# Performance work log

Hardware: AMD Instinct MI355X
Metric: run time of the kernel (lower is better)

The kernel has to match this reference:

```python
import jax, jax.numpy as jnp
import numpy as np

N_NODES = 50000
N_EDGES = 800000
VOCAB = 15000
IN_FEATS = 128
HIDDEN = 32
HEADS = 4
N_GRAPHS = 64
NEG_SLOPE = 0.2


def setup_inputs() -> dict:
    key = jax.random.key(0)
    ks = jax.random.split(key, 16)
    word_ids = jax.random.randint(ks[0], (N_NODES,), 0, VOCAB)
    edge_src = jax.random.randint(ks[1], (N_EDGES,), 0, N_NODES)
    edge_dst = jax.random.randint(ks[2], (N_EDGES,), 0, N_NODES)
    node_graph_id = jnp.sort(jax.random.randint(ks[3], (N_NODES,), 0, N_GRAPHS))
    y_data = jax.random.uniform(ks[4], (N_GRAPHS,))
    word_embeds = jax.random.normal(ks[5], (VOCAB, IN_FEATS)) * 0.02
    W0 = jax.random.normal(ks[6], (IN_FEATS, HEADS * HIDDEN)) * (1.0 / np.sqrt(IN_FEATS))
    al0 = jax.random.normal(ks[7], (HEADS, HIDDEN)) * 0.1
    ar0 = jax.random.normal(ks[8], (HEADS, HIDDEN)) * 0.1
    W1 = jax.random.normal(ks[9], (HEADS * HIDDEN, HEADS * HIDDEN)) * (1.0 / np.sqrt(HEADS * HIDDEN))
    al1 = jax.random.normal(ks[10], (HEADS, HIDDEN)) * 0.1
    ar1 = jax.random.normal(ks[11], (HEADS, HIDDEN)) * 0.1
    out_w = jax.random.normal(ks[12], (HEADS * HIDDEN, 1)) * (1.0 / np.sqrt(HEADS * HIDDEN))
    out_b = jnp.zeros((1,))
    return {"word_ids": word_ids, "edge_src": edge_src, "edge_dst": edge_dst,
            "node_graph_id": node_graph_id, "y_data": y_data,
            "word_embeds": word_embeds, "W0": W0, "al0": al0, "ar0": ar0,
            "W1": W1, "al1": al1, "ar1": ar1, "out_w": out_w, "out_b": out_b}


def gat_layer(h, src, dst, W, al, ar):
    # h: [N, Fin] -> feat: [N, H, D]
    feat = (h @ W).reshape(N_NODES, HEADS, HIDDEN)
    el = (feat * al[None]).sum(-1)  # [N, H]
    er = (feat * ar[None]).sum(-1)  # [N, H]
    e = jax.nn.leaky_relu(el[src] + er[dst], NEG_SLOPE)  # [E, H]
    # segment softmax over incoming edges of each dst node
    m = jax.ops.segment_max(e, dst, num_segments=N_NODES)
    m = jnp.where(jnp.isfinite(m), m, 0.0)
    ex = jnp.exp(e - m[dst])
    denom = jax.ops.segment_sum(ex, dst, num_segments=N_NODES)
    alpha = ex / (denom[dst] + 1e-10)  # [E, H]
    msg = feat[src] * alpha[:, :, None]  # [E, H, D]
    out = jax.ops.segment_sum(msg, dst, num_segments=N_NODES)  # [N, H, D]
    return jax.nn.elu(out).reshape(N_NODES, HEADS * HIDDEN)


def reference(word_ids, edge_src, edge_dst, node_graph_id, y_data,
              word_embeds, W0, al0, ar0, W1, al1, ar1, out_w, out_b):
    h = word_embeds[word_ids]  # [N, IN_FEATS]
    h = gat_layer(h, edge_src, edge_dst, W0, al0, ar0)
    h = gat_layer(h, edge_src, edge_dst, W1, al1, ar1)
    # per-graph max pooling over nodes
    pooled = jax.ops.segment_max(h, node_graph_id, num_segments=N_GRAPHS)
    pooled = jnp.where(jnp.isfinite(pooled), pooled, 0.0)  # guard empty graphs
    logits = (pooled @ out_w + out_b).reshape(-1)  # [G]
    # BCE with logits (stable)
    loss = jnp.mean(jnp.maximum(logits, 0.0) - logits * y_data
                    + jnp.log1p(jnp.exp(-jnp.abs(logits))))
    y_pred = jax.nn.sigmoid(logits)[:, None]
    return (loss, y_pred)
```

## Files before the change

kernel.cpp:

```cpp
#include <hip/hip_runtime.h>
#include <math.h>

#define N_NODES 50000
#define N_EDGES 800000
#define HEADS 4
#define N_GRAPHS 64
#define NEG_SLOPE 0.2f
#define LOG2E 1.4426950408889634f
#define SCAN_NB 196
#define POOL_CHUNK 200
#define POOL_NB 250
#define FEAT_NB 1563
#define EDGE_Q 200000
#define EDGE_NB 782

__device__ __forceinline__ unsigned fkey(float f) {
    unsigned u = __float_as_uint(f);
    return (u & 0x80000000u) ? ~u : (u | 0x80000000u);
}
__device__ __forceinline__ float kval(unsigned k) {
    unsigned u = (k & 0x80000000u) ? (k & 0x7FFFFFFFu) : ~k;
    return __uint_as_float(u);
}

__device__ __forceinline__ unsigned short f2bf(float f) {
    unsigned u = __float_as_uint(f);
    u += 0x7FFFu + ((u >> 16) & 1u);
    return (unsigned short)(u >> 16);
}
__device__ __forceinline__ unsigned pack_bf2(float a, float b) {
    return (unsigned)f2bf(a) | ((unsigned)f2bf(b) << 16);
}


__global__ void hist_kernel(const int* __restrict__ dst, int* __restrict__ deg,
                            int* __restrict__ rank) {
    int i = blockIdx.x * 256 + threadIdx.x;
    if (i >= EDGE_Q) return;
    int e0 = i, e1 = i + EDGE_Q, e2 = i + 2 * EDGE_Q, e3 = i + 3 * EDGE_Q;
    int d0 = dst[e0], d1 = dst[e1], d2 = dst[e2], d3 = dst[e3];
    int r0 = atomicAdd(&deg[d0], 1);
    int r1 = atomicAdd(&deg[d1], 1);
    int r2 = atomicAdd(&deg[d2], 1);
    int r3 = atomicAdd(&deg[d3], 1);
    rank[e0] = r0; rank[e1] = r1; rank[e2] = r2; rank[e3] = r3;
}

__global__ void partial_kernel(const int* __restrict__ deg, int* __restrict__ partial) {
    int t = threadIdx.x, b = blockIdx.x;
    int i = b * 256 + t;
    int v = (i < N_NODES) ? deg[i] : 0;
    #pragma unroll
    for (int off = 1; off < 64; off <<= 1) v += __shfl_xor(v, off, 64);
    __shared__ int wsum[4];
    if ((t & 63) == 0) wsum[t >> 6] = v;
    __syncthreads();
    if (t == 0) partial[b] = wsum[0] + wsum[1] + wsum[2] + wsum[3];
}

__global__ void csr_offsets_kernel(const int* __restrict__ deg, const int* __restrict__ partial,
                                   int* __restrict__ row_start) {
    __shared__ int sb[SCAN_NB];
    __shared__ int wsumA[4];
    __shared__ int wsumB[4];
    int t = threadIdx.x, b = blockIdx.x;
    int lane = t & 63, w = t >> 6;
    {
        int v = (t < SCAN_NB) ? partial[t] : 0;
        int incl = v;
        #pragma unroll
        for (int off = 1; off < 64; off <<= 1) {
            int u = __shfl_up(incl, off, 64);
            if (lane >= off) incl += u;
        }
        if (lane == 63) wsumA[w] = incl;
        __syncthreads();
        int woff = 0;
        #pragma unroll
        for (int k = 0; k < 4; ++k) if (k < w) woff += wsumA[k];
        if (t < SCAN_NB) sb[t] = woff + incl - v;
        __syncthreads();
    }
    int i = b * 256 + t;
    int v = (i < N_NODES) ? deg[i] : 0;
    int incl = v;
    #pragma unroll
    for (int off = 1; off < 64; off <<= 1) {
        int u = __shfl_up(incl, off, 64);
        if (lane >= off) incl += u;
    }
    if (lane == 63) wsumB[w] = incl;
    __syncthreads();
    int woff = sb[b];
    #pragma unroll
    for (int k = 0; k < 4; ++k) if (k < w) woff += wsumB[k];
    int excl = woff + incl - v;
    if (i < N_NODES) row_start[i] = excl;
    else if (i == N_NODES) row_start[i] = excl;
}

__global__ void scatter_kernel(const int* __restrict__ src, const int* __restrict__ dst,
                               const int* __restrict__ rank, const int* __restrict__ row_start,
                               int* __restrict__ csr_src) {
    int i = blockIdx.x * 256 + threadIdx.x;
    if (i >= EDGE_Q) return;
    int e0 = i, e1 = i + EDGE_Q, e2 = i + 2 * EDGE_Q, e3 = i + 3 * EDGE_Q;
    int d0 = dst[e0], d1 = dst[e1], d2 = dst[e2], d3 = dst[e3];
    int k0 = rank[e0], k1 = rank[e1], k2 = rank[e2], k3 = rank[e3];
    int s0 = src[e0], s1 = src[e1], s2 = src[e2], s3 = src[e3];
    int p0 = row_start[d0] + k0;
    int p1 = row_start[d1] + k1;
    int p2 = row_start[d2] + k2;
    int p3 = row_start[d3] + k3;
    csr_src[p0] = s0;
    csr_src[p1] = s1;
    csr_src[p2] = s2;
    csr_src[p3] = s3;
}


__global__ __launch_bounds__(256, 2)
void feat_kernel(const float* __restrict__ h, const int* __restrict__ wid,
                 const float* __restrict__ W,
                 const float* __restrict__ al, const float* __restrict__ ar,
                 unsigned* __restrict__ featb, float* __restrict__ el,
                 float* __restrict__ er) {
    __shared__ float Wl[128 * 128];
    __shared__ float hl[32 * 128];
    int t = threadIdx.x;
    {
        const float4* W4 = (const float4*)W;
        float4* Wl4 = (float4*)Wl;
        #pragma unroll
        for (int i = 0; i < 16; ++i) Wl4[t + 256 * i] = W4[t + 256 * i];
    }
    int n0 = blockIdx.x * 32;
    {
        const float4* h4 = (const float4*)h;
        float4* hl4 = (float4*)hl;
        #pragma unroll
        for (int r = 0; r < 4; ++r) {
            int i = t + 256 * r;
            int n = i >> 5, q = i & 31;
            float4 v = {0.f, 0.f, 0.f, 0.f};
            int gn = n0 + n;
            if (gn < N_NODES) {
                int row = wid ? wid[gn] : gn;
                v = h4[(size_t)row * 32 + q];
            }
            hl4[n * 32 + q] = v;
        }
    }
    __syncthreads();
    int ng = t >> 5, cg = t & 31;
    const float4* hl4 = (const float4*)hl;
    const float4* Wl4 = (const float4*)Wl;
    float4 acc[4];
    #pragma unroll
    for (int i = 0; i < 4; ++i) acc[i] = {0.f, 0.f, 0.f, 0.f};
    for (int k4 = 0; k4 < 32; ++k4) {
        float4 a0 = hl4[(ng * 4 + 0) * 32 + k4];
        float4 a1 = hl4[(ng * 4 + 1) * 32 + k4];
        float4 a2 = hl4[(ng * 4 + 2) * 32 + k4];
        float4 a3 = hl4[(ng * 4 + 3) * 32 + k4];
        #pragma unroll
        for (int kk = 0; kk < 4; ++kk) {
            float4 w = Wl4[(k4 * 4 + kk) * 32 + cg];
            float c0 = ((const float*)&a0)[kk];
            float c1 = ((const float*)&a1)[kk];
            float c2 = ((const float*)&a2)[kk];
            float c3 = ((const float*)&a3)[kk];
            acc[0].x += c0 * w.x; acc[0].y += c0 * w.y; acc[0].z += c0 * w.z; acc[0].w += c0 * w.w;
            acc[1].x += c1 * w.x; acc[1].y += c1 * w.y; acc[1].z += c1 * w.z; acc[1].w += c1 * w.w;
            acc[2].x += c2 * w.x; acc[2].y += c2 * w.y; acc[2].z += c2 * w.z; acc[2].w += c2 * w.w;
            acc[3].x += c3 * w.x; acc[3].y += c3 * w.y; acc[3].z += c3 * w.z; acc[3].w += c3 * w.w;
        }
    }
    int hd = cg >> 3;
    float a0v = al[cg * 4], a1v = al[cg * 4 + 1], a2v = al[cg * 4 + 2], a3v = al[cg * 4 + 3];
    float r0v = ar[cg * 4], r1v = ar[cg * 4 + 1], r2v = ar[cg * 4 + 2], r3v = ar[cg * 4 + 3];
    #pragma unroll
    for (int i = 0; i < 4; ++i) {
        int n = n0 + ng * 4 + i;
        if (n >= N_NODES) break;
        uint2 pk;
        pk.x = pack_bf2(acc[i].x, acc[i].y);
        pk.y = pack_bf2(acc[i].z, acc[i].w);
        *(uint2*)(featb + (size_t)n * 64 + cg * 2) = pk;
        float pl = acc[i].x * a0v + acc[i].y * a1v + acc[i].z * a2v + acc[i].w * a3v;
        float pr = acc[i].x * r0v + acc[i].y * r1v + acc[i].z * r2v + acc[i].w * r3v;
        #pragma unroll
        for (int off = 1; off < 8; off <<= 1) {
            pl += __shfl_xor(pl, off, 64);
            pr += __shfl_xor(pr, off, 64);
        }
        if ((t & 7) == 0) {
            el[n * 4 + hd] = pl * LOG2E;
            er[n * 4 + hd] = pr * LOG2E;
        }
    }
}

__global__ void gat_aggregate(const int* __restrict__ row_start, const int* __restrict__ csr_src,
                              const unsigned* __restrict__ featb, const float* __restrict__ el,
                              const float* __restrict__ er, float* __restrict__ hout) {
    int lane = threadIdx.x & 63;
    int d = blockIdx.x * 4 + (threadIdx.x >> 6);
    int beg = row_start[d], end = row_start[d + 1];
    int eg = lane >> 4;
    int li = lane & 15;
    int hc = li >> 2;
    float er_h = er[d * 4 + hc];
    float a0 = 0.f, a1 = 0.f, a2 = 0.f, a3 = 0.f;
    float a4 = 0.f, a5 = 0.f, a6 = 0.f, a7 = 0.f;
    float dsum = 0.f;
    int b8 = beg + ((end - beg) & ~7);
    for (int base = beg; base < b8; base += 8) {
        int ea = base + eg, eb = base + 4 + eg;
        int sa = csr_src[ea];
        int sb = csr_src[eb];
        float la = el[sa * 4 + hc];
        float lb = el[sb * 4 + hc];
        uint4 pa = *(const uint4*)(featb + (size_t)sa * 64 + li * 4);
        uint4 pb = *(const uint4*)(featb + (size_t)sb * 64 + li * 4);
        float va = la + er_h; va = fmaxf(va, NEG_SLOPE * va);
        float vb = lb + er_h; vb = fmaxf(vb, NEG_SLOPE * vb);
        float xa = exp2f(va), xb = exp2f(vb);
        dsum += xa + xb;
        a0 += __uint_as_float(pa.x << 16) * xa;
        a1 += __uint_as_float(pa.x & 0xFFFF0000u) * xa;
        a2 += __uint_as_float(pa.y << 16) * xa;
        a3 += __uint_as_float(pa.y & 0xFFFF0000u) * xa;
        a4 += __uint_as_float(pa.z << 16) * xa;
        a5 += __uint_as_float(pa.z & 0xFFFF0000u) * xa;
        a6 += __uint_as_float(pa.w << 16) * xa;
        a7 += __uint_as_float(pa.w & 0xFFFF0000u) * xa;
        a0 += __uint_as_float(pb.x << 16) * xb;
        a1 += __uint_as_float(pb.x & 0xFFFF0000u) * xb;
        a2 += __uint_as_float(pb.y << 16) * xb;
        a3 += __uint_as_float(pb.y & 0xFFFF0000u) * xb;
        a4 += __uint_as_float(pb.z << 16) * xb;
        a5 += __uint_as_float(pb.z & 0xFFFF0000u) * xb;
        a6 += __uint_as_float(pb.w << 16) * xb;
        a7 += __uint_as_float(pb.w & 0xFFFF0000u) * xb;
    }
    for (int ee = b8 + eg; ee < end; ee += 4) {
        int s = csr_src[ee];
        float lv = el[s * 4 + hc];
        uint4 pv = *(const uint4*)(featb + (size_t)s * 64 + li * 4);
        float v = lv + er_h; v = fmaxf(v, NEG_SLOPE * v);
        float x = exp2f(v);
        dsum += x;
        a0 += __uint_as_float(pv.x << 16) * x;
        a1 += __uint_as_float(pv.x & 0xFFFF0000u) * x;
        a2 += __uint_as_float(pv.y << 16) * x;
        a3 += __uint_as_float(pv.y & 0xFFFF0000u) * x;
        a4 += __uint_as_float(pv.z << 16) * x;
        a5 += __uint_as_float(pv.z & 0xFFFF0000u) * x;
        a6 += __uint_as_float(pv.w << 16) * x;
        a7 += __uint_as_float(pv.w & 0xFFFF0000u) * x;
    }
    #pragma unroll
    for (int off = 16; off < 64; off <<= 1) {
        a0 += __shfl_xor(a0, off, 64);
        a1 += __shfl_xor(a1, off, 64);
        a2 += __shfl_xor(a2, off, 64);
        a3 += __shfl_xor(a3, off, 64);
        a4 += __shfl_xor(a4, off, 64);
        a5 += __shfl_xor(a5, off, 64);
        a6 += __shfl_xor(a6, off, 64);
        a7 += __shfl_xor(a7, off, 64);
        dsum += __shfl_xor(dsum, off, 64);
    }
    if (eg == 0) {
        float inv = 1.f / (dsum + 1e-10f);
        float o0 = a0 * inv, o1 = a1 * inv, o2 = a2 * inv, o3 = a3 * inv;
        float o4 = a4 * inv, o5 = a5 * inv, o6 = a6 * inv, o7 = a7 * inv;
        o0 = o0 > 0.f ? o0 : expm1f(o0);
        o1 = o1 > 0.f ? o1 : expm1f(o1);
        o2 = o2 > 0.f ? o2 : expm1f(o2);
        o3 = o3 > 0.f ? o3 : expm1f(o3);
        o4 = o4 > 0.f ? o4 : expm1f(o4);
        o5 = o5 > 0.f ? o5 : expm1f(o5);
        o6 = o6 > 0.f ? o6 : expm1f(o6);
        o7 = o7 > 0.f ? o7 : expm1f(o7);
        float4* op = (float4*)(hout + (size_t)d * 128);
        float4 w0 = {o0, o1, o2, o3};
        float4 w1 = {o4, o5, o6, o7};
        op[li * 2] = w0;
        op[li * 2 + 1] = w1;
    }
}


__global__ void pool_kernel(const int* __restrict__ gid, const float* __restrict__ h,
                            unsigned* __restrict__ pkeys) {
    int t = threadIdx.x;
    int c = t & 127;
    int par = t >> 7;
    int n0 = blockIdx.x * POOL_CHUNK;
    float m = 0.f;
    int cur_g = -1;
    for (int n = n0 + par; n < n0 + POOL_CHUNK; n += 2) {
        int g = gid[n];
        if (g != cur_g) {
            if (cur_g >= 0) atomicMax(&pkeys[cur_g * 128 + c], fkey(m));
            cur_g = g;
            m = -3.0e38f;
        }
        m = fmaxf(m, h[(size_t)n * 128 + c]);
    }
    if (cur_g >= 0) atomicMax(&pkeys[cur_g * 128 + c], fkey(m));
}

__global__ void logits_kernel(const unsigned* __restrict__ pkeys, const float* __restrict__ w,
                              const float* __restrict__ bptr, float* __restrict__ logits) {
    int g = blockIdx.x, t = threadIdx.x;
    float sum = 0.f;
    for (int c = t; c < 128; c += 64) {
        unsigned k = pkeys[g * 128 + c];
        float v = (k == 0u) ? 0.f : kval(k);
        sum += v * w[c];
    }
    #pragma unroll
    for (int off = 32; off; off >>= 1) sum += __shfl_down(sum, off, 64);
    if (t == 0) logits[g] = sum + bptr[0];
}

__global__ void final_kernel(const float* __restrict__ logits, const float* __restrict__ y,
                             float* __restrict__ out) {
    int t = threadIdx.x;
    float l = logits[t];
    float term = fmaxf(l, 0.f) - l * y[t] + log1pf(expf(-fabsf(l)));
    float s = term;
    #pragma unroll
    for (int off = 32; off; off >>= 1) s += __shfl_down(s, off, 64);
    out[1 + t] = 1.f / (1.f + expf(-l));
    if (t == 0) out[0] = s * (1.f / 64.f);
}

extern "C" void kernel_launch(void* const* d_in, const int* in_sizes, int n_in,
                              void* d_out, int out_size, void* d_ws, size_t ws_size,
                              hipStream_t stream) {
    const int* word_ids  = (const int*)d_in[0];
    const int* esrc      = (const int*)d_in[1];
    const int* edst      = (const int*)d_in[2];
    const int* gid       = (const int*)d_in[3];
    const float* y_data  = (const float*)d_in[4];
    const float* emb     = (const float*)d_in[5];
    const float* W0      = (const float*)d_in[6];
    const float* al0     = (const float*)d_in[7];
    const float* ar0     = (const float*)d_in[8];
    const float* W1      = (const float*)d_in[9];
    const float* al1     = (const float*)d_in[10];
    const float* ar1     = (const float*)d_in[11];
    const float* out_w   = (const float*)d_in[12];
    const float* out_b   = (const float*)d_in[13];
    float* out = (float*)d_out;

    float* ws = (float*)d_ws;
    unsigned* featb  = (unsigned*)ws;
    float*    hbuf   = ws + 3200000;
    float*    el     = ws + 9600000;
    float*    er     = ws + 9800000;
    int*      row_st = (int*)(ws + 10000000);
    int*      deg    = (int*)(ws + 10051000);
    int*      rank   = (int*)(ws + 10101000);
    int*      csrsrc = (int*)(ws + 10901000);
    int*      partial= (int*)(ws + 11701000);
    unsigned* pkeys  = (unsigned*)(ws + 11701400);
    float*    logits = ws + 11709592;

    hipMemsetAsync(deg, 0, (size_t)N_NODES * 4, stream);
    hist_kernel<<<EDGE_NB, 256, 0, stream>>>(edst, deg, rank);
    partial_kernel<<<SCAN_NB, 256, 0, stream>>>(deg, partial);
    csr_offsets_kernel<<<SCAN_NB, 256, 0, stream>>>(deg, partial, row_st);
    scatter_kernel<<<EDGE_NB, 256, 0, stream>>>(esrc, edst, rank, row_st, csrsrc);

    feat_kernel<<<FEAT_NB, 256, 0, stream>>>(emb, word_ids, W0, al0, ar0, featb, el, er);
    gat_aggregate<<<12500, 256, 0, stream>>>(row_st, csrsrc, featb, el, er, hbuf);
    feat_kernel<<<FEAT_NB, 256, 0, stream>>>(hbuf, nullptr, W1, al1, ar1, featb, el, er);
    gat_aggregate<<<12500, 256, 0, stream>>>(row_st, csrsrc, featb, el, er, hbuf);

    hipMemsetAsync(pkeys, 0, (size_t)N_GRAPHS * 128 * 4, stream);
    pool_kernel<<<POOL_NB, 256, 0, stream>>>(gid, hbuf, pkeys);
    logits_kernel<<<N_GRAPHS, 64, 0, stream>>>(pkeys, out_w, out_b, logits);
    final_kernel<<<1, 64, 0, stream>>>(logits, y_data, out);
}
```

Baseline: 329.4 us.

## Compute GAT feature projection with bf16 MFMA using pre-packed weight fragments

Replaces the FP32 FMA matmul in feat_kernel with bf16 MFMA 16x16x32 instructions. A small wfrag_kernel first repacks W into bf16 fragment order, so the feature kernel no longer stages the full 64KB FP32 weight matrix in LDS for every block. Each block now handles 64 nodes and fewer blocks are launched. Node features are also rounded to bf16 before the multiply, which lowers precision, and the el/er head reductions are reworked to fit the MFMA output layout.

```diff
diff --git a/kernel.cpp b/kernel.cpp
--- a/kernel.cpp
+++ b/kernel.cpp
@@ -10,9 +10,12 @@
 #define SCAN_NB 196
 #define POOL_CHUNK 200
 #define POOL_NB 250
-#define FEAT_NB 1563
+#define FEAT_NB 782
 #define EDGE_Q 200000
 #define EDGE_NB 782
+
+typedef __attribute__((ext_vector_type(8))) short bf16x8;
+typedef __attribute__((ext_vector_type(4))) float f32x4;
 
 __device__ __forceinline__ unsigned fkey(float f) {
     unsigned u = __float_as_uint(f);
@@ -108,95 +111,105 @@
     int d0 = dst[e0], d1 = dst[e1], d2 = dst[e2], d3 = dst[e3];
     int k0 = rank[e0], k1 = rank[e1], k2 = rank[e2], k3 = rank[e3];
     int s0 = src[e0], s1 = src[e1], s2 = src[e2], s3 = src[e3];
-    int p0 = row_start[d0] + k0;
-    int p1 = row_start[d1] + k1;
-    int p2 = row_start[d2] + k2;
-    int p3 = row_start[d3] + k3;
-    csr_src[p0] = s0;
-    csr_src[p1] = s1;
-    csr_src[p2] = s2;
-    csr_src[p3] = s3;
-}
-
-
-__global__ __launch_bounds__(256, 2)
+    csr_src[row_start[d0] + k0] = s0;
+    csr_src[row_start[d1] + k1] = s1;
+    csr_src[row_start[d2] + k2] = s2;
+    csr_src[row_start[d3] + k3] = s3;
+}
+
+
+__global__ void wfrag_kernel(const float* __restrict__ W, unsigned* __restrict__ wf) {
+    int slot = blockIdx.x * 256 + threadIdx.x;
+    int f = slot >> 6, l = slot & 63;
+    int n = l & 15, q = l >> 4;
+    int ct = f >> 2, kq = f & 3;
+    int col = 16 * ct + n;
+    int k0 = 32 * kq + 8 * q;
+    uint4 o;
+    o.x = pack_bf2(W[(k0 + 0) * 128 + col], W[(k0 + 1) * 128 + col]);
+    o.y = pack_bf2(W[(k0 + 2) * 128 + col], W[(k0 + 3) * 128 + col]);
+    o.z = pack_bf2(W[(k0 + 4) * 128 + col], W[(k0 + 5) * 128 + col]);
+    o.w = pack_bf2(W[(k0 + 6) * 128 + col], W[(k0 + 7) * 128 + col]);
+    ((uint4*)wf)[slot] = o;
+}
+
+__global__ __launch_bounds__(256)
 void feat_kernel(const float* __restrict__ h, const int* __restrict__ wid,
-                 const float* __restrict__ W,
+                 const unsigned* __restrict__ wf,
                  const float* __restrict__ al, const float* __restrict__ ar,
                  unsigned* __restrict__ featb, float* __restrict__ el,
                  float* __restrict__ er) {
-    __shared__ float Wl[128 * 128];
-    __shared__ float hl[32 * 128];
+    __shared__ unsigned hl[64 * 68];
     int t = threadIdx.x;
-    {
-        const float4* W4 = (const float4*)W;
-        float4* Wl4 = (float4*)Wl;
+    int n0 = blockIdx.x * 64;
+    const float4* h4 = (const float4*)h;
+    #pragma unroll
+    for (int r = 0; r < 8; ++r) {
+        int i = t + 256 * r;
+        int n = i >> 5, q4 = i & 31;
+        float4 v = {0.f, 0.f, 0.f, 0.f};
+        int gn = n0 + n;
+        if (gn < N_NODES) {
+            int row = wid ? wid[gn] : gn;
+            v = h4[(size_t)row * 32 + q4];
+        }
+        hl[n * 68 + q4 * 2]     = pack_bf2(v.x, v.y);
+        hl[n * 68 + q4 * 2 + 1] = pack_bf2(v.z, v.w);
+    }
+    __syncthreads();
+    int w = t >> 6, lane = t & 63;
+    int col = lane & 15, quad = lane >> 4;
+    int nbase = n0 + 16 * w;
+    bf16x8 afr[4];
+    #pragma unroll
+    for (int kq = 0; kq < 4; ++kq)
+        afr[kq] = *(const bf16x8*)&hl[(16 * w + col) * 68 + 16 * kq + 4 * quad];
+    f32x4 acc[8];
+    #pragma unroll
+    for (int ct = 0; ct < 8; ++ct) acc[ct] = (f32x4){0.f, 0.f, 0.f, 0.f};
+    const uint4* wf4 = (const uint4*)wf;
+    #pragma unroll
+    for (int ct = 0; ct < 8; ++ct) {
         #pragma unroll
-        for (int i = 0; i < 16; ++i) Wl4[t + 256 * i] = W4[t + 256 * i];
-    }
-    int n0 = blockIdx.x * 32;
-    {
-        const float4* h4 = (const float4*)h;
-        float4* hl4 = (float4*)hl;
+        for (int kq = 0; kq < 4; ++kq) {
+            uint4 braw = wf4[(ct * 4 + kq) * 64 + lane];
+            bf16x8 bfr = *(const bf16x8*)&braw;
+            acc[ct] = __builtin_amdgcn_mfma_f32_16x16x32_bf16(afr[kq], bfr, acc[ct], 0, 0, 0);
+        }
+    }
+    #pragma unroll
+    for (int ct = 0; ct < 8; ++ct) {
         #pragma unroll
-        for (int r = 0; r < 4; ++r) {
-            int i = t + 256 * r;
-            int n = i >> 5, q = i & 31;
-            float4 v = {0.f, 0.f, 0.f, 0.f};
-            int gn = n0 + n;
-            if (gn < N_NODES) {
-                int row = wid ? wid[gn] : gn;
-                v = h4[(size_t)row * 32 + q];
+        for (int reg = 0; reg < 4; ++reg) {
+            float v = acc[ct][reg];
+            float pv = __shfl_xor(v, 1, 64);
+            int node = nbase + quad * 4 + reg;
+            if (!(col & 1) && node < N_NODES)
+                featb[(size_t)node * 64 + ct * 8 + (col >> 1)] = pack_bf2(v, pv);
+        }
+    }
+    float alv[8], arv[8];
+    #pragma unroll
+    for (int ct = 0; ct < 8; ++ct) {
+        alv[ct] = al[ct * 16 + col];
+        arv[ct] = ar[ct * 16 + col];
+    }
+    #pragma unroll
+    for (int reg = 0; reg < 4; ++reg) {
+        int node = nbase + quad * 4 + reg;
+        #pragma unroll
+        for (int hd = 0; hd < 4; ++hd) {
+            float pl = acc[2 * hd][reg] * alv[2 * hd] + acc[2 * hd + 1][reg] * alv[2 * hd + 1];
+            float pr = acc[2 * hd][reg] * arv[2 * hd] + acc[2 * hd + 1][reg] * arv[2 * hd + 1];
+            #pragma unroll
+            for (int off = 1; off < 16; off <<= 1) {
+                pl += __shfl_xor(pl, off, 64);
+                pr += __shfl_xor(pr, off, 64);
             }
-            hl4[n * 32 + q] = v;
-        }
-    }
-    __syncthreads();
-    int ng = t >> 5, cg = t & 31;
-    const float4* hl4 = (const float4*)hl;
-    const float4* Wl4 = (const float4*)Wl;
-    float4 acc[4];
-    #pragma unroll
-    for (int i = 0; i < 4; ++i) acc[i] = {0.f, 0.f, 0.f, 0.f};
-    for (int k4 = 0; k4 < 32; ++k4) {
-        float4 a0 = hl4[(ng * 4 + 0) * 32 + k4];
-        float4 a1 = hl4[(ng * 4 + 1) * 32 + k4];
-        float4 a2 = hl4[(ng * 4 + 2) * 32 + k4];
-        float4 a3 = hl4[(ng * 4 + 3) * 32 + k4];
-        #pragma unroll
-        for (int kk = 0; kk < 4; ++kk) {
-            float4 w = Wl4[(k4 * 4 + kk) * 32 + cg];
-            float c0 = ((const float*)&a0)[kk];
-            float c1 = ((const float*)&a1)[kk];
-            float c2 = ((const float*)&a2)[kk];
-            float c3 = ((const float*)&a3)[kk];
-            acc[0].x += c0 * w.x; acc[0].y += c0 * w.y; acc[0].z += c0 * w.z; acc[0].w += c0 * w.w;
-            acc[1].x += c1 * w.x; acc[1].y += c1 * w.y; acc[1].z += c1 * w.z; acc[1].w += c1 * w.w;
-            acc[2].x += c2 * w.x; acc[2].y += c2 * w.y; acc[2].z += c2 * w.z; acc[2].w += c2 * w.w;
-            acc[3].x += c3 * w.x; acc[3].y += c3 * w.y; acc[3].z += c3 * w.z; acc[3].w += c3 * w.w;
-        }
-    }
-    int hd = cg >> 3;
-    float a0v = al[cg * 4], a1v = al[cg * 4 + 1], a2v = al[cg * 4 + 2], a3v = al[cg * 4 + 3];
-    float r0v = ar[cg * 4], r1v = ar[cg * 4 + 1], r2v = ar[cg * 4 + 2], r3v = ar[cg * 4 + 3];
-    #pragma unroll
-    for (int i = 0; i < 4; ++i) {
-        int n = n0 + ng * 4 + i;
-        if (n >= N_NODES) break;
-        uint2 pk;
-        pk.x = pack_bf2(acc[i].x, acc[i].y);
-        pk.y = pack_bf2(acc[i].z, acc[i].w);
-        *(uint2*)(featb + (size_t)n * 64 + cg * 2) = pk;
-        float pl = acc[i].x * a0v + acc[i].y * a1v + acc[i].z * a2v + acc[i].w * a3v;
-        float pr = acc[i].x * r0v + acc[i].y * r1v + acc[i].z * r2v + acc[i].w * r3v;
-        #pragma unroll
-        for (int off = 1; off < 8; off <<= 1) {
-            pl += __shfl_xor(pl, off, 64);
-            pr += __shfl_xor(pr, off, 64);
-        }
-        if ((t & 7) == 0) {
-            el[n * 4 + hd] = pl * LOG2E;
-            er[n * 4 + hd] = pr * LOG2E;
+            if (col == hd && node < N_NODES) {
+                el[node * 4 + hd] = pl * LOG2E;
+                er[node * 4 + hd] = pr * LOG2E;
+            }
         }
     }
 }
@@ -370,6 +383,7 @@
     int*      partial= (int*)(ws + 11701000);
     unsigned* pkeys  = (unsigned*)(ws + 11701400);
     float*    logits = ws + 11709592;
+    unsigned* wfbuf  = (unsigned*)(ws + 11709704);
 
     hipMemsetAsync(deg, 0, (size_t)N_NODES * 4, stream);
     hist_kernel<<<EDGE_NB, 256, 0, stream>>>(edst, deg, rank);
@@ -377,9 +391,11 @@
     csr_offsets_kernel<<<SCAN_NB, 256, 0, stream>>>(deg, partial, row_st);
     scatter_kernel<<<EDGE_NB, 256, 0, stream>>>(esrc, edst, rank, row_st, csrsrc);
 
-    feat_kernel<<<FEAT_NB, 256, 0, stream>>>(emb, word_ids, W0, al0, ar0, featb, el, er);
+    wfrag_kernel<<<8, 256, 0, stream>>>(W0, wfbuf);
+    feat_kernel<<<FEAT_NB, 256, 0, stream>>>(emb, word_ids, wfbuf, al0, ar0, featb, el, er);
     gat_aggregate<<<12500, 256, 0, stream>>>(row_st, csrsrc, featb, el, er, hbuf);
-    feat_kernel<<<FEAT_NB, 256, 0, stream>>>(hbuf, nullptr, W1, al1, ar1, featb, el, er);
+    wfrag_kernel<<<8, 256, 0, stream>>>(W1, wfbuf);
+    feat_kernel<<<FEAT_NB, 256, 0, stream>>>(hbuf, nullptr, wfbuf, al1, ar1, featb, el, er);
     gat_aggregate<<<12500, 256, 0, stream>>>(row_st, csrsrc, featb, el, er, hbuf);
 
     hipMemsetAsync(pkeys, 0, (size_t)N_GRAPHS * 128 * 4, stream);
```

Result: faster. 299.3 us (-9.1%).
